# Performance work log

Measured on AMD Instinct MI355X. Metric: run time of the kernel, lower is better.

The kernel has to match this reference:

```python
import jax, jax.numpy as jnp
import numpy as np

SEQ_LEN = 8192
HEAD_DIM = 128


def setup_inputs() -> dict:
    key = jax.random.key(0)
    kq, kk, kv = jax.random.split(key, 3)
    q = jax.random.normal(kq, (SEQ_LEN, HEAD_DIM), dtype=jnp.float32)
    k = jax.random.normal(kk, (SEQ_LEN, HEAD_DIM), dtype=jnp.float32)
    v = jax.random.normal(kv, (SEQ_LEN, HEAD_DIM), dtype=jnp.float32)
    return {"q": q, "k": k, "v": v}


def reference(q, k, v):
    # FlashAttention computes exact softmax attention; the blocked loops with
    # online max/sum rescaling in the source are an exact reformulation of:
    #   O = softmax(Q K^T) V
    # NOTE: the original module applies no 1/sqrt(d) scaling, so neither do we.
    s = jnp.einsum('nd,md->nm', q, k)          # [N, N] scores
    p = jax.nn.softmax(s, axis=-1)             # stable softmax (online in src)
    return jnp.einsum('nm,md->nd', p, v)       # [N, d]
```

## Files before the change

### kernel.cpp

```cpp
#include <hip/hip_runtime.h>

#define N_SEQ 8192
#define HDIM  128

typedef _Float16 half8v  __attribute__((ext_vector_type(8)));
typedef float    floatx16 __attribute__((ext_vector_type(16)));
typedef unsigned int uint32;

__global__ void prep_kv(const float* __restrict__ K, const float* __restrict__ V,
                        _Float16* __restrict__ K16s, _Float16* __restrict__ Vs) {
    __shared__ float Kl[32 * 132];
    __shared__ float Vl[32 * 132];
    const int t  = threadIdx.x;
    const int nt = blockIdx.x;
    const int n0 = nt * 32;
    #pragma unroll
    for (int kk = 0; kk < 4; kk++) {
        int idx = t + 256 * kk;
        int nl = idx >> 5, c4 = idx & 31;
        float4 f = *(((const float4*)(K + (size_t)(n0 + nl) * HDIM)) + c4);
        float* dk = &Kl[nl * 132 + c4 * 4];
        dk[0] = f.x; dk[1] = f.y; dk[2] = f.z; dk[3] = f.w;
        float4 g = *(((const float4*)(V + (size_t)(n0 + nl) * HDIM)) + c4);
        float* dv = &Vl[nl * 132 + c4 * 4];
        dv[0] = g.x; dv[1] = g.y; dv[2] = g.z; dv[3] = g.w;
    }
    __syncthreads();
    #pragma unroll
    for (int rep = 0; rep < 2; rep++) {
        int ch = t + rep * 256;
        int kc = ch >> 6, lane = ch & 63, l31 = lane & 31, q5 = (lane >> 5) & 1;
        half8v h;
        #pragma unroll
        for (int j = 0; j < 8; j++) h[j] = (_Float16)Kl[l31 * 132 + kc * 16 + q5 * 8 + j];
        *(half8v*)(K16s + (((size_t)nt * 8 + kc) * 64 + lane) * 8) = h;
    }
    #pragma unroll
    for (int rep = 0; rep < 2; rep++) {
        int ch = t + rep * 256;
        int dt = ch >> 7, kc2 = (ch >> 6) & 1, lane = ch & 63, l31 = lane & 31, q5 = (lane >> 5) & 1;
        half8v h;
        #pragma unroll
        for (int j = 0; j < 8; j++) h[j] = (_Float16)Vl[(kc2 * 16 + q5 * 8 + j) * 132 + dt * 32 + l31];
        *(half8v*)(Vs + ((((size_t)nt * 4 + dt) * 2 + kc2) * 64 + lane) * 8) = h;
    }
}

static __device__ __forceinline__ void stage_tile(
        const _Float16* __restrict__ K16s, const _Float16* __restrict__ Vs,
        _Float16* lds, size_t nt, int wv, int lane) {
    #pragma unroll
    for (int i = 0; i < 4; i++) {
        const int c = wv * 4 + i;
        const _Float16* base = (c < 8) ? (K16s + (nt * 8 + c) * 512)
                                       : (Vs + (nt * 8 + (size_t)(c - 8)) * 512);
        __builtin_amdgcn_global_load_lds(
            (const __attribute__((address_space(1))) void*)(base + lane * 8),
            (__attribute__((address_space(3))) void*)(lds + c * 512),
            16, 0, 0);
    }
}

static __device__ __forceinline__ void do_pv(const half8v (&vsrc)[8], const uint32 (&hpk)[8],
                                             floatx16 (&oacc)[4], int q5) {
    #pragma unroll
    for (int kc2 = 0; kc2 < 2; kc2++) {
        uint32 pass0 = q5 ? hpk[4 * kc2 + 0] : hpk[4 * kc2 + 2];
        uint32 pass1 = q5 ? hpk[4 * kc2 + 1] : hpk[4 * kc2 + 3];
        uint32 r0 = (uint32)__shfl_xor((int)pass0, 32, 64);
        uint32 r1 = (uint32)__shfl_xor((int)pass1, 32, 64);
        uint32 b0 = q5 ? r0 : hpk[4 * kc2 + 0];
        uint32 b1 = q5 ? r1 : hpk[4 * kc2 + 1];
        uint32 b2 = q5 ? hpk[4 * kc2 + 2] : r0;
        uint32 b3 = q5 ? hpk[4 * kc2 + 3] : r1;
        uint4 bu = make_uint4(b0, b1, b2, b3);
        half8v bfrag = __builtin_bit_cast(half8v, bu);
        #pragma unroll
        for (int dt = 0; dt < 4; dt++)
            oacc[dt] = __builtin_amdgcn_mfma_f32_32x32x16_f16(vsrc[dt * 2 + kc2], bfrag, oacc[dt], 0, 0, 0);
    }
}

static __device__ __forceinline__ void step64(
        const half8v (&qf)[8], floatx16 (&oacc)[4],
        float& runm, float& lsum,
        const _Float16* lds, int lane, int q5) {
    half8v kf[8];
    #pragma unroll
    for (int kc = 0; kc < 8; kc++)
        kf[kc] = *(const half8v*)(lds + kc * 512 + lane * 8);
    floatx16 s0, s1;
    #pragma unroll
    for (int r = 0; r < 16; r++) { s0[r] = 0.0f; s1[r] = 0.0f; }
    #pragma unroll
    for (int kc = 0; kc < 4; kc++)
        s0 = __builtin_amdgcn_mfma_f32_32x32x16_f16(kf[kc], qf[kc], s0, 0, 0, 0);
    #pragma unroll
    for (int kc = 4; kc < 8; kc++)
        s1 = __builtin_amdgcn_mfma_f32_32x32x16_f16(kf[kc], qf[kc], s1, 0, 0, 0);
    float sA[16];
    #pragma unroll
    for (int r = 0; r < 16; r++) sA[r] = s0[r] + s1[r];
    #pragma unroll
    for (int kc = 0; kc < 8; kc++)
        kf[kc] = *(const half8v*)(lds + 8192 + kc * 512 + lane * 8);
    #pragma unroll
    for (int r = 0; r < 16; r++) { s0[r] = 0.0f; s1[r] = 0.0f; }
    #pragma unroll
    for (int kc = 0; kc < 4; kc++)
        s0 = __builtin_amdgcn_mfma_f32_32x32x16_f16(kf[kc], qf[kc], s0, 0, 0, 0);
    #pragma unroll
    for (int kc = 4; kc < 8; kc++)
        s1 = __builtin_amdgcn_mfma_f32_32x32x16_f16(kf[kc], qf[kc], s1, 0, 0, 0);
    float sB[16];
    #pragma unroll
    for (int r = 0; r < 16; r++) sB[r] = s0[r] + s1[r];
    float tm[8];
    #pragma unroll
    for (int r = 0; r < 8; r++)
        tm[r] = fmaxf(fmaxf(sA[r], sA[r + 8]), fmaxf(sB[r], sB[r + 8]));
    #pragma unroll
    for (int w = 4; w; w >>= 1)
        #pragma unroll
        for (int r = 0; r < w; r++) tm[r] = fmaxf(tm[r], tm[r + w]);
    float cmax = fmaxf(tm[0], __shfl_xor(tm[0], 32, 64));
    if (__any(cmax > runm + 12.0f)) {
        const float mnew = fmaxf(runm, cmax);
        const float alpha = __builtin_amdgcn_exp2f(runm - mnew);
        #pragma unroll
        for (int dt = 0; dt < 4; dt++)
            #pragma unroll
            for (int r = 0; r < 16; r++) oacc[dt][r] *= alpha;
        lsum *= alpha;
        runm = mnew;
    }
    float pA[16], pB[16];
    #pragma unroll
    for (int r = 0; r < 16; r++) pA[r] = __builtin_amdgcn_exp2f(sA[r] - runm);
    #pragma unroll
    for (int r = 0; r < 16; r++) pB[r] = __builtin_amdgcn_exp2f(sB[r] - runm);
    float ts[8];
    #pragma unroll
    for (int r = 0; r < 8; r++) ts[r] = (pA[r] + pA[r + 8]) + (pB[r] + pB[r + 8]);
    #pragma unroll
    for (int w = 4; w; w >>= 1)
        #pragma unroll
        for (int r = 0; r < w; r++) ts[r] += ts[r + w];
    lsum += ts[0];
    uint32 hA[8], hB[8];
    #pragma unroll
    for (int t2 = 0; t2 < 8; t2++) {
        auto ka = __builtin_amdgcn_cvt_pkrtz(pA[2 * t2], pA[2 * t2 + 1]);
        hA[t2] = __builtin_bit_cast(uint32, ka);
        auto kb = __builtin_amdgcn_cvt_pkrtz(pB[2 * t2], pB[2 * t2 + 1]);
        hB[t2] = __builtin_bit_cast(uint32, kb);
    }
    #pragma unroll
    for (int j = 0; j < 8; j++)
        kf[j] = *(const half8v*)(lds + (8 + j) * 512 + lane * 8);
    do_pv(kf, hA, oacc, q5);
    #pragma unroll
    for (int j = 0; j < 8; j++)
        kf[j] = *(const half8v*)(lds + 8192 + (8 + j) * 512 + lane * 8);
    do_pv(kf, hB, oacc, q5);
}

__launch_bounds__(256, 2)
__global__ void fa_main(const float* __restrict__ Qp, const _Float16* __restrict__ K16s,
                        const _Float16* __restrict__ Vs, float* __restrict__ Opart,
                        float* __restrict__ lpart, float* __restrict__ mpart, int tiles) {
    __shared__ _Float16 ldsbuf[2][16384];
    const int tid  = threadIdx.x;
    const int lane = tid & 63;
    const int wv   = tid >> 6;
    const int l31  = lane & 31;
    const int q5   = lane >> 5;
    const int sp   = blockIdx.x;
    const int m0   = blockIdx.y * 128 + wv * 32;
    const float LOG2E = 1.44269504088896f;

    half8v qf[8];
    {
        const float* qrow = Qp + (size_t)(m0 + l31) * HDIM;
        #pragma unroll
        for (int kc = 0; kc < 8; kc++) {
            const float4 a = *(const float4*)(qrow + kc * 16 + q5 * 8);
            const float4 b = *(const float4*)(qrow + kc * 16 + q5 * 8 + 4);
            half8v h;
            h[0] = (_Float16)(a.x * LOG2E); h[1] = (_Float16)(a.y * LOG2E);
            h[2] = (_Float16)(a.z * LOG2E); h[3] = (_Float16)(a.w * LOG2E);
            h[4] = (_Float16)(b.x * LOG2E); h[5] = (_Float16)(b.y * LOG2E);
            h[6] = (_Float16)(b.z * LOG2E); h[7] = (_Float16)(b.w * LOG2E);
            qf[kc] = h;
        }
    }

    floatx16 oacc[4];
    #pragma unroll
    for (int dt = 0; dt < 4; dt++)
        #pragma unroll
        for (int r = 0; r < 16; r++) oacc[dt][r] = 0.0f;

    float runm = -3.0e38f;
    float lsum = 0.0f;

    const size_t nt0 = (size_t)sp * tiles;
    const int phases = tiles >> 1;

    stage_tile(K16s, Vs, ldsbuf[0], nt0 + 0, wv, lane);
    stage_tile(K16s, Vs, ldsbuf[0] + 8192, nt0 + 1, wv, lane);
    __syncthreads();
    for (int ph = 0; ph < phases; ph++) {
        _Float16* cur = ldsbuf[ph & 1];
        _Float16* nxt = ldsbuf[(ph & 1) ^ 1];
        if (ph + 1 < phases) {
            stage_tile(K16s, Vs, nxt, nt0 + 2 * ph + 2, wv, lane);
            stage_tile(K16s, Vs, nxt + 8192, nt0 + 2 * ph + 3, wv, lane);
        }
        step64(qf, oacc, runm, lsum, cur, lane, q5);
        __syncthreads();
    }

    float ltot = lsum + __shfl_xor(lsum, 32, 64);
    if (lane < 32) {
        lpart[(size_t)sp * N_SEQ + m0 + l31] = ltot;
        mpart[(size_t)sp * N_SEQ + m0 + l31] = runm;
    }

    float* ldsf = (float*)ldsbuf;
    const size_t obase = ((size_t)sp * N_SEQ + blockIdx.y * 128) * HDIM;
    #pragma unroll
    for (int qtr = 0; qtr < 4; qtr++) {
        __syncthreads();
        if (wv == qtr) {
            #pragma unroll
            for (int dt = 0; dt < 4; dt++)
                #pragma unroll
                for (int g = 0; g < 4; g++) {
                    float4 v = make_float4(oacc[dt][4 * g + 0], oacc[dt][4 * g + 1],
                                           oacc[dt][4 * g + 2], oacc[dt][4 * g + 3]);
                    *(float4*)&ldsf[l31 * 132 + dt * 32 + g * 8 + q5 * 4] = v;
                }
        }
        __syncthreads();
        const int lrow = wv * 8 + (lane >> 3);
        const int c    = lane & 7;
        #pragma unroll
        for (int j = 0; j < 4; j++) {
            float4 v = *(const float4*)&ldsf[lrow * 132 + (j * 8 + c) * 4];
            *(float4*)&Opart[obase + (size_t)(qtr * 32 + lrow) * HDIM + (j * 8 + c) * 4] = v;
        }
    }
}

template <int S>
__global__ __launch_bounds__(256) void fa_merge(const float* __restrict__ Opart,
                                                const float* __restrict__ lpart,
                                                const float* __restrict__ mpart,
                                                float* __restrict__ Out) {
    const int t = threadIdx.x;
    const int m = blockIdx.x * 16 + (t >> 4);
    const int c = t & 15;

    float mv[S], lv[S];
    #pragma unroll
    for (int s = 0; s < S; s++) {
        mv[s] = mpart[(size_t)s * N_SEQ + m];
        lv[s] = lpart[(size_t)s * N_SEQ + m];
    }
    float M = -3.0e38f;
    #pragma unroll
    for (int s = 0; s < S; s++) M = fmaxf(M, mv[s]);
    float wsc[S];
    float L = 0.0f;
    #pragma unroll
    for (int s = 0; s < S; s++) {
        wsc[s] = __builtin_amdgcn_exp2f(mv[s] - M);
        L += lv[s] * wsc[s];
    }
    const float inv = 1.0f / L;

    float4 acc[2];
    #pragma unroll
    for (int j = 0; j < 2; j++) acc[j] = make_float4(0.f, 0.f, 0.f, 0.f);
    #pragma unroll
    for (int s = 0; s < S; s++) {
        const float ww = wsc[s] * inv;
        const float* src = Opart + ((size_t)s * N_SEQ + m) * HDIM;
        #pragma unroll
        for (int j = 0; j < 2; j++) {
            float4 v = *(const float4*)&src[(j * 16 + c) * 4];
            acc[j].x += v.x * ww; acc[j].y += v.y * ww;
            acc[j].z += v.z * ww; acc[j].w += v.w * ww;
        }
    }
    float* dst = Out + (size_t)m * HDIM;
    #pragma unroll
    for (int j = 0; j < 2; j++)
        *(float4*)&dst[(j * 16 + c) * 4] = acc[j];
}

__global__ void fa_naive(const float* __restrict__ Q, const float* __restrict__ K,
                         const float* __restrict__ V, float* __restrict__ O) {
    const int m = blockIdx.x;
    const int t = threadIdx.x;
    __shared__ float qs[HDIM];
    __shared__ float ps[256];
    __shared__ float red[256];
    if (t < HDIM) qs[t] = Q[(size_t)m * HDIM + t] * 1.44269504f;
    __syncthreads();
    float om = -3.0e38f, ls = 0.0f, oa = 0.0f;
    for (int nb = 0; nb < N_SEQ; nb += 256) {
        const float* kr = K + (size_t)(nb + t) * HDIM;
        float s = 0.0f;
        #pragma unroll 8
        for (int d = 0; d < HDIM; d++) s += qs[d] * kr[d];
        red[t] = s; __syncthreads();
        for (int st = 128; st > 0; st >>= 1) { if (t < st) red[t] = fmaxf(red[t], red[t + st]); __syncthreads(); }
        float cm = red[0];
        __syncthreads();
        float mn = fmaxf(om, cm);
        float al = __builtin_amdgcn_exp2f(om - mn);
        om = mn;
        float pp = __builtin_amdgcn_exp2f(s - mn);
        ps[t] = pp; red[t] = pp; __syncthreads();
        for (int st = 128; st > 0; st >>= 1) { if (t < st) red[t] += red[t + st]; __syncthreads(); }
        float csum = red[0];
        ls = ls * al + csum;
        if (t < HDIM) {
            float acc = 0.0f;
            for (int j = 0; j < 256; j++) acc += ps[j] * V[(size_t)(nb + j) * HDIM + t];
            oa = oa * al + acc;
        }
        __syncthreads();
    }
    if (t < HDIM) O[(size_t)m * HDIM + t] = oa / ls;
}

extern "C" void kernel_launch(void* const* d_in, const int* in_sizes, int n_in,
                              void* d_out, int out_size, void* d_ws, size_t ws_size,
                              hipStream_t stream) {
    const float* q = (const float*)d_in[0];
    const float* k = (const float*)d_in[1];
    const float* v = (const float*)d_in[2];
    float* out = (float*)d_out;

    const size_t MB = 1024ull * 1024ull;
    int S = 0;
    for (int s = 8; s >= 1; s >>= 1) {
        size_t need = 4 * MB + (size_t)s * (4 * MB + 64 * 1024);
        if (ws_size >= need) { S = s; break; }
    }
    if (S == 0) {
        fa_naive<<<N_SEQ, 256, 0, stream>>>(q, k, v, out);
        return;
    }
    char* ws = (char*)d_ws;
    _Float16* K16s = (_Float16*)ws;
    _Float16* Vs   = (_Float16*)(ws + 2 * MB);
    float* Opart   = (float*)(ws + 4 * MB);
    float* lpart   = (float*)(ws + 4 * MB + (size_t)S * 4 * MB);
    float* mpart   = lpart + (size_t)S * N_SEQ;

    prep_kv<<<dim3(N_SEQ / 32), dim3(256), 0, stream>>>(k, v, K16s, Vs);
    fa_main<<<dim3(S, N_SEQ / 128), dim3(256), 0, stream>>>(q, K16s, Vs, Opart, lpart, mpart, (N_SEQ / 32) / S);
    dim3 mg(N_SEQ / 16);
    switch (S) {
        case 8:  fa_merge<8> <<<mg, dim3(256), 0, stream>>>(Opart, lpart, mpart, out); break;
        case 4:  fa_merge<4> <<<mg, dim3(256), 0, stream>>>(Opart, lpart, mpart, out); break;
        case 2:  fa_merge<2> <<<mg, dim3(256), 0, stream>>>(Opart, lpart, mpart, out); break;
        default: fa_merge<1> <<<mg, dim3(256), 0, stream>>>(Opart, lpart, mpart, out); break;
    }
}
```

Before: 119.5 us.

## Process one 32-key tile per step, raise occupancy, allow 12-way KV split

The main loop now handles a single 32-key tile per iteration instead of two, which halves the shared-memory double buffer and the score and probability registers. With that smaller footprint the launch bounds ask for three blocks per multiprocessor. The key range is split unevenly across a grid dimension that can now be 12 splits, with a matching merge instantiation, to fill more compute units. The cost is twice as many barriers and online-softmax rescale checks per key, and a merge over more partial outputs.

```diff
diff --git a/kernel.cpp b/kernel.cpp
--- a/kernel.cpp
+++ b/kernel.cpp
@@ -81,7 +81,7 @@
     }
 }
 
-static __device__ __forceinline__ void step64(
+static __device__ __forceinline__ void step32(
         const half8v (&qf)[8], floatx16 (&oacc)[4],
         float& runm, float& lsum,
         const _Float16* lds, int lane, int q5) {
@@ -98,27 +98,12 @@
     #pragma unroll
     for (int kc = 4; kc < 8; kc++)
         s1 = __builtin_amdgcn_mfma_f32_32x32x16_f16(kf[kc], qf[kc], s1, 0, 0, 0);
-    float sA[16];
-    #pragma unroll
-    for (int r = 0; r < 16; r++) sA[r] = s0[r] + s1[r];
-    #pragma unroll
-    for (int kc = 0; kc < 8; kc++)
-        kf[kc] = *(const half8v*)(lds + 8192 + kc * 512 + lane * 8);
-    #pragma unroll
-    for (int r = 0; r < 16; r++) { s0[r] = 0.0f; s1[r] = 0.0f; }
-    #pragma unroll
-    for (int kc = 0; kc < 4; kc++)
-        s0 = __builtin_amdgcn_mfma_f32_32x32x16_f16(kf[kc], qf[kc], s0, 0, 0, 0);
-    #pragma unroll
-    for (int kc = 4; kc < 8; kc++)
-        s1 = __builtin_amdgcn_mfma_f32_32x32x16_f16(kf[kc], qf[kc], s1, 0, 0, 0);
-    float sB[16];
-    #pragma unroll
-    for (int r = 0; r < 16; r++) sB[r] = s0[r] + s1[r];
+    float sc[16];
+    #pragma unroll
+    for (int r = 0; r < 16; r++) sc[r] = s0[r] + s1[r];
     float tm[8];
     #pragma unroll
-    for (int r = 0; r < 8; r++)
-        tm[r] = fmaxf(fmaxf(sA[r], sA[r + 8]), fmaxf(sB[r], sB[r + 8]));
+    for (int r = 0; r < 8; r++) tm[r] = fmaxf(sc[r], sc[r + 8]);
     #pragma unroll
     for (int w = 4; w; w >>= 1)
         #pragma unroll
@@ -134,48 +119,41 @@
         lsum *= alpha;
         runm = mnew;
     }
-    float pA[16], pB[16];
-    #pragma unroll
-    for (int r = 0; r < 16; r++) pA[r] = __builtin_amdgcn_exp2f(sA[r] - runm);
-    #pragma unroll
-    for (int r = 0; r < 16; r++) pB[r] = __builtin_amdgcn_exp2f(sB[r] - runm);
+    float p[16];
+    #pragma unroll
+    for (int r = 0; r < 16; r++) p[r] = __builtin_amdgcn_exp2f(sc[r] - runm);
     float ts[8];
     #pragma unroll
-    for (int r = 0; r < 8; r++) ts[r] = (pA[r] + pA[r + 8]) + (pB[r] + pB[r + 8]);
+    for (int r = 0; r < 8; r++) ts[r] = p[r] + p[r + 8];
     #pragma unroll
     for (int w = 4; w; w >>= 1)
         #pragma unroll
         for (int r = 0; r < w; r++) ts[r] += ts[r + w];
     lsum += ts[0];
-    uint32 hA[8], hB[8];
+    uint32 hpk[8];
     #pragma unroll
     for (int t2 = 0; t2 < 8; t2++) {
-        auto ka = __builtin_amdgcn_cvt_pkrtz(pA[2 * t2], pA[2 * t2 + 1]);
-        hA[t2] = __builtin_bit_cast(uint32, ka);
-        auto kb = __builtin_amdgcn_cvt_pkrtz(pB[2 * t2], pB[2 * t2 + 1]);
-        hB[t2] = __builtin_bit_cast(uint32, kb);
+        auto pk = __builtin_amdgcn_cvt_pkrtz(p[2 * t2], p[2 * t2 + 1]);
+        hpk[t2] = __builtin_bit_cast(uint32, pk);
     }
     #pragma unroll
     for (int j = 0; j < 8; j++)
         kf[j] = *(const half8v*)(lds + (8 + j) * 512 + lane * 8);
-    do_pv(kf, hA, oacc, q5);
-    #pragma unroll
-    for (int j = 0; j < 8; j++)
-        kf[j] = *(const half8v*)(lds + 8192 + (8 + j) * 512 + lane * 8);
-    do_pv(kf, hB, oacc, q5);
-}
-
-__launch_bounds__(256, 2)
+    do_pv(kf, hpk, oacc, q5);
+}
+
+__launch_bounds__(256, 3)
 __global__ void fa_main(const float* __restrict__ Qp, const _Float16* __restrict__ K16s,
                         const _Float16* __restrict__ Vs, float* __restrict__ Opart,
-                        float* __restrict__ lpart, float* __restrict__ mpart, int tiles) {
-    __shared__ _Float16 ldsbuf[2][16384];
+                        float* __restrict__ lpart, float* __restrict__ mpart, int ntile) {
+    __shared__ _Float16 ldsbuf[2][8192];
     const int tid  = threadIdx.x;
     const int lane = tid & 63;
     const int wv   = tid >> 6;
     const int l31  = lane & 31;
     const int q5   = lane >> 5;
     const int sp   = blockIdx.x;
+    const int S    = gridDim.x;
     const int m0   = blockIdx.y * 128 + wv * 32;
     const float LOG2E = 1.44269504088896f;
 
@@ -204,20 +182,17 @@
     float runm = -3.0e38f;
     float lsum = 0.0f;
 
-    const size_t nt0 = (size_t)sp * tiles;
-    const int phases = tiles >> 1;
-
-    stage_tile(K16s, Vs, ldsbuf[0], nt0 + 0, wv, lane);
-    stage_tile(K16s, Vs, ldsbuf[0] + 8192, nt0 + 1, wv, lane);
+    const int t0  = (sp * ntile) / S;
+    const int t1  = ((sp + 1) * ntile) / S;
+    const int cnt = t1 - t0;
+
+    stage_tile(K16s, Vs, ldsbuf[0], t0, wv, lane);
     __syncthreads();
-    for (int ph = 0; ph < phases; ph++) {
+    for (int ph = 0; ph < cnt; ph++) {
         _Float16* cur = ldsbuf[ph & 1];
         _Float16* nxt = ldsbuf[(ph & 1) ^ 1];
-        if (ph + 1 < phases) {
-            stage_tile(K16s, Vs, nxt, nt0 + 2 * ph + 2, wv, lane);
-            stage_tile(K16s, Vs, nxt + 8192, nt0 + 2 * ph + 3, wv, lane);
-        }
-        step64(qf, oacc, runm, lsum, cur, lane, q5);
+        if (ph + 1 < cnt) stage_tile(K16s, Vs, nxt, (size_t)(t0 + ph + 1), wv, lane);
+        step32(qf, oacc, runm, lsum, cur, lane, q5);
         __syncthreads();
     }
 
@@ -346,8 +321,10 @@
     float* out = (float*)d_out;
 
     const size_t MB = 1024ull * 1024ull;
+    const int cand[5] = {12, 8, 4, 2, 1};
     int S = 0;
-    for (int s = 8; s >= 1; s >>= 1) {
+    for (int i = 0; i < 5; i++) {
+        int s = cand[i];
         size_t need = 4 * MB + (size_t)s * (4 * MB + 64 * 1024);
         if (ws_size >= need) { S = s; break; }
     }
@@ -363,9 +340,10 @@
     float* mpart   = lpart + (size_t)S * N_SEQ;
 
     prep_kv<<<dim3(N_SEQ / 32), dim3(256), 0, stream>>>(k, v, K16s, Vs);
-    fa_main<<<dim3(S, N_SEQ / 128), dim3(256), 0, stream>>>(q, K16s, Vs, Opart, lpart, mpart, (N_SEQ / 32) / S);
+    fa_main<<<dim3(S, N_SEQ / 128), dim3(256), 0, stream>>>(q, K16s, Vs, Opart, lpart, mpart, N_SEQ / 32);
     dim3 mg(N_SEQ / 16);
     switch (S) {
+        case 12: fa_merge<12><<<mg, dim3(256), 0, stream>>>(Opart, lpart, mpart, out); break;
         case 8:  fa_merge<8> <<<mg, dim3(256), 0, stream>>>(Opart, lpart, mpart, out); break;
         case 4:  fa_merge<4> <<<mg, dim3(256), 0, stream>>>(Opart, lpart, mpart, out); break;
         case 2:  fa_merge<2> <<<mg, dim3(256), 0, stream>>>(Opart, lpart, mpart, out); break;
```

Measured after the change: 124.0 us. 3.8% more time.
